# Optimization experiments

Hardware: AMD Instinct MI355X
Metric: run time of the kernel (lower is better)

The kernel has to match this reference:

```python
import jax, jax.numpy as jnp
import numpy as np

EPS = 1e-5

def conv2d(x, w, b):
    # x: [B,C,H,W], w: [O,I,kh,kw], VALID padding, stride 1
    y = jax.lax.conv_general_dilated(x, w, (1, 1), 'VALID',
                                     dimension_numbers=('NCHW', 'OIHW', 'NCHW'))
    return y + b[None, :, None, None]

def batchnorm(x, g, b):
    # training-mode BN: batch statistics over (N,H,W), biased variance (torch semantics)
    m = jnp.mean(x, axis=(0, 2, 3), keepdims=True)
    v = jnp.mean((x - m) ** 2, axis=(0, 2, 3), keepdims=True)
    return g[None, :, None, None] * (x - m) / jnp.sqrt(v + EPS) + b[None, :, None, None]

def maxpool2(x):
    return jax.lax.reduce_window(x, -jnp.inf, jax.lax.max,
                                 (1, 1, 2, 2), (1, 1, 2, 2), 'VALID')

def self_attention(x, qw, qb, kw, kb, vw, vb, gamma):
    # x: [B,C,H,W]; qw/kw: [C//8, C]; vw: [C, C] (1x1 convs)
    B, C, H, W = x.shape
    xf = x.reshape(B, C, H * W)                               # [B,C,N]
    q = jnp.einsum('oc,bcn->bon', qw, xf) + qb[None, :, None]  # [B,C//8,N]
    k = jnp.einsum('oc,bcn->bon', kw, xf) + kb[None, :, None]
    v = jnp.einsum('oc,bcn->bon', vw, xf) + vb[None, :, None]  # [B,C,N]
    energy = jnp.einsum('bcn,bcm->bnm', q, k)                  # [B,N,N] (query n, key m)
    attn = jax.nn.softmax(energy, axis=-1)
    out = jnp.einsum('bcm,bnm->bcn', v, attn)                  # [B,C,N]
    return gamma * out.reshape(B, C, H, W) + x

def setup_inputs() -> dict:
    key = jax.random.key(0)
    ks = jax.random.split(key, 20)
    s = 0.05
    d = {}
    d['x'] = jax.random.normal(ks[0], (1, 3, 256, 256), jnp.float32)
    d['conv1_w'] = jax.random.normal(ks[1], (32, 3, 3, 3), jnp.float32) * s
    d['conv1_b'] = jnp.zeros((32,), jnp.float32)
    d['bn1_g'] = jnp.ones((32,), jnp.float32)
    d['bn1_b'] = jnp.zeros((32,), jnp.float32)
    d['a1_qw'] = jax.random.normal(ks[2], (4, 32), jnp.float32) * s
    d['a1_qb'] = jnp.zeros((4,), jnp.float32)
    d['a1_kw'] = jax.random.normal(ks[3], (4, 32), jnp.float32) * s
    d['a1_kb'] = jnp.zeros((4,), jnp.float32)
    d['a1_vw'] = jax.random.normal(ks[4], (32, 32), jnp.float32) * s
    d['a1_vb'] = jnp.zeros((32,), jnp.float32)
    d['a1_gamma'] = jnp.ones((1,), jnp.float32)
    d['conv2_w'] = jax.random.normal(ks[5], (64, 32, 3, 3), jnp.float32) * s
    d['conv2_b'] = jnp.zeros((64,), jnp.float32)
    d['bn2_g'] = jnp.ones((64,), jnp.float32)
    d['bn2_b'] = jnp.zeros((64,), jnp.float32)
    d['a2_qw'] = jax.random.normal(ks[6], (8, 64), jnp.float32) * s
    d['a2_qb'] = jnp.zeros((8,), jnp.float32)
    d['a2_kw'] = jax.random.normal(ks[7], (8, 64), jnp.float32) * s
    d['a2_kb'] = jnp.zeros((8,), jnp.float32)
    d['a2_vw'] = jax.random.normal(ks[8], (64, 64), jnp.float32) * s
    d['a2_vb'] = jnp.zeros((64,), jnp.float32)
    d['a2_gamma'] = jnp.ones((1,), jnp.float32)
    d['fc_w'] = jax.random.normal(ks[9], (50, 64 * 62 * 62), jnp.float32) * 0.002
    d['fc_b'] = jnp.zeros((50,), jnp.float32)
    return d

def reference(x, conv1_w, conv1_b, bn1_g, bn1_b,
              a1_qw, a1_qb, a1_kw, a1_kb, a1_vw, a1_vb, a1_gamma,
              conv2_w, conv2_b, bn2_g, bn2_b,
              a2_qw, a2_qb, a2_kw, a2_kb, a2_vw, a2_vb, a2_gamma,
              fc_w, fc_b):
    h = conv2d(x, conv1_w, conv1_b)                 # [B,32,254,254]
    h = jax.nn.relu(batchnorm(h, bn1_g, bn1_b))
    h = maxpool2(h)                                 # [B,32,127,127]
    h = self_attention(h, a1_qw, a1_qb, a1_kw, a1_kb, a1_vw, a1_vb, a1_gamma)
    h = conv2d(h, conv2_w, conv2_b)                 # [B,64,125,125]
    h = jax.nn.relu(batchnorm(h, bn2_g, bn2_b))
    h = maxpool2(h)                                 # [B,64,62,62]
    h = self_attention(h, a2_qw, a2_qb, a2_kw, a2_kb, a2_vw, a2_vb, a2_gamma)
    h = h.reshape(h.shape[0], -1)                   # [B, 64*62*62]
    return h @ fc_w.T + fc_b
```

## Files before the change

### kernel.cpp

```cpp
#include <hip/hip_runtime.h>
#include <hip/hip_bf16.h>

typedef float f32x4 __attribute__((ext_vector_type(4)));
typedef short bf16x8 __attribute__((ext_vector_type(8)));

__device__ inline unsigned short f2bf(float x) {
    __hip_bfloat16 h = __float2bfloat16(x);
    return *reinterpret_cast<unsigned short*>(&h);
}

__global__ void conv3x3_kernel(const float* __restrict__ src, int Cin, int H, int W,
                               const float* __restrict__ w, const float* __restrict__ b,
                               float* __restrict__ dst, int OH, int OW) {
    extern __shared__ float lds[];
    float* xs = lds;
    float* ws = lds + Cin * 324;
    const int oc  = blockIdx.z;
    const int tx0 = blockIdx.x * 16, ty0 = blockIdx.y * 16;
    const int tid = threadIdx.y * 16 + threadIdx.x;

    for (int i = tid; i < Cin * 9; i += 256) ws[i] = w[oc * Cin * 9 + i];
    for (int i = tid; i < Cin * 324; i += 256) {
        int ic = i / 324;
        int r  = (i % 324) / 18;
        int cc = (i % 324) % 18;
        int y = ty0 + r, x = tx0 + cc;
        xs[i] = (y < H && x < W) ? src[((size_t)ic * H + y) * W + x] : 0.f;
    }
    __syncthreads();

    const int ox = tx0 + threadIdx.x, oy = ty0 + threadIdx.y;
    if (ox >= OW || oy >= OH) return;
    float acc = b[oc];
    for (int ic = 0; ic < Cin; ++ic) {
        const float* xp = &xs[ic * 324 + threadIdx.y * 18 + threadIdx.x];
        const float* wp = &ws[ic * 9];
        #pragma unroll
        for (int kh = 0; kh < 3; ++kh)
            #pragma unroll
            for (int kw = 0; kw < 3; ++kw)
                acc += xp[kh * 18 + kw] * wp[kh * 3 + kw];
    }
    dst[((size_t)oc * OH + oy) * OW + ox] = acc;
}

__global__ void bn_part_kernel(const float* __restrict__ src, int spatial,
                               float* __restrict__ part) {
    const int c = blockIdx.x, sb = blockIdx.y, SB = gridDim.y;
    const float* p = src + (size_t)c * spatial;
    const int nv4 = spatial >> 2;
    const int per = (nv4 + SB - 1) / SB;
    const int j0 = sb * per, j1 = min(nv4, j0 + per);
    float s = 0.f, sq = 0.f;
    const float4* p4 = (const float4*)p;
    for (int j = j0 + (int)threadIdx.x; j < j1; j += 256) {
        float4 x = p4[j];
        s  += x.x + x.y + x.z + x.w;
        sq += x.x * x.x + x.y * x.y + x.z * x.z + x.w * x.w;
    }
    if (sb == 0) {
        for (int j = (nv4 << 2) + (int)threadIdx.x; j < spatial; j += 256) {
            float x = p[j]; s += x; sq += x * x;
        }
    }
    __shared__ float rs[256], rq[256];
    rs[threadIdx.x] = s; rq[threadIdx.x] = sq;
    __syncthreads();
    for (int off = 128; off > 0; off >>= 1) {
        if ((int)threadIdx.x < off) {
            rs[threadIdx.x] += rs[threadIdx.x + off];
            rq[threadIdx.x] += rq[threadIdx.x + off];
        }
        __syncthreads();
    }
    if (threadIdx.x == 0) {
        part[(c * SB + sb) * 2]     = rs[0];
        part[(c * SB + sb) * 2 + 1] = rq[0];
    }
}

__global__ void bn_final_kernel(const float* __restrict__ part, int SB, int spatial,
                                const float* __restrict__ g, const float* __restrict__ bb,
                                float* __restrict__ inv_shift) {
    int c = blockIdx.x;
    if (threadIdx.x != 0) return;
    float s = 0.f, sq = 0.f;
    for (int i = 0; i < SB; ++i) {
        s  += part[(c * SB + i) * 2];
        sq += part[(c * SB + i) * 2 + 1];
    }
    float m   = s / (float)spatial;
    float var = sq / (float)spatial - m * m;
    float inv = g[c] * rsqrtf(var + 1e-5f);
    inv_shift[c * 2]     = inv;
    inv_shift[c * 2 + 1] = bb[c] - m * inv;
}

__global__ void bn_pool_kernel(const float* __restrict__ src,
                               const float* __restrict__ inv_shift,
                               int H, int W, int OH, int OW, int C,
                               float* __restrict__ dst) {
    int i = blockIdx.x * blockDim.x + threadIdx.x;
    if (i >= C * OH * OW) return;
    int ox = i % OW;
    int oy = (i / OW) % OH;
    int c  = i / (OW * OH);
    float inv = inv_shift[c * 2], sh = inv_shift[c * 2 + 1];
    const float* p = src + ((size_t)c * H + 2 * oy) * W + 2 * ox;
    float a = fmaxf(fmaf(p[0],     inv, sh), 0.f);
    float b = fmaxf(fmaf(p[1],     inv, sh), 0.f);
    float d = fmaxf(fmaf(p[W],     inv, sh), 0.f);
    float e = fmaxf(fmaf(p[W + 1], inv, sh), 0.f);
    dst[i] = fmaxf(fmaxf(a, b), fmaxf(d, e));
}

__global__ void qkv_proj_kernel(const float* __restrict__ xf, int N, int NP, int C, int Cqk,
                                const float* __restrict__ qw, const float* __restrict__ qb,
                                const float* __restrict__ kw, const float* __restrict__ kb,
                                const float* __restrict__ vw, const float* __restrict__ vb,
                                float* __restrict__ q, float* __restrict__ k,
                                unsigned short* __restrict__ v) {
    constexpr int OCG = 8;
    __shared__ float wl[OCG * 64 + OCG];
    const int g0 = blockIdx.y * OCG;
    const int tid = threadIdx.x;
    for (int i = tid; i < OCG * C; i += blockDim.x) {
        int o = i / C, cc = i % C;
        int oc = g0 + o;
        const float* wsrc = (oc < Cqk) ? (qw + oc * C)
                          : (oc < 2 * Cqk) ? (kw + (oc - Cqk) * C)
                          : (vw + (oc - 2 * Cqk) * C);
        wl[o * C + cc] = wsrc[cc];
    }
    if (tid < OCG) {
        int oc = g0 + tid;
        wl[OCG * C + tid] = (oc < Cqk) ? qb[oc]
                          : (oc < 2 * Cqk) ? kb[oc - Cqk]
                          : vb[oc - 2 * Cqk];
    }
    __syncthreads();
    int n = blockIdx.x * blockDim.x + tid;
    if (n >= N) return;
    float acc[OCG];
    #pragma unroll
    for (int o = 0; o < OCG; ++o) acc[o] = wl[OCG * C + o];
    for (int c = 0; c < C; ++c) {
        float xv = xf[(size_t)c * N + n];
        #pragma unroll
        for (int o = 0; o < OCG; ++o) acc[o] += xv * wl[o * C + c];
    }
    #pragma unroll
    for (int o = 0; o < OCG; ++o) {
        int oc = g0 + o;
        if (oc < Cqk)            q[(size_t)oc * NP + n] = acc[o];
        else if (oc < 2 * Cqk)   k[(size_t)(oc - Cqk) * NP + n] = acc[o];
        else                     v[(size_t)(oc - 2 * Cqk) * NP + n] = f2bf(acc[o]);
    }
}

template <int CQK, int CV>
__launch_bounds__(256)
__global__ void flash_mfma_kernel(const float* __restrict__ q,
                                  const float* __restrict__ k,
                                  const unsigned short* __restrict__ v,
                                  int N, int NP, int chunk,
                                  float* __restrict__ l_part,
                                  float* __restrict__ acc_part) {
    __shared__ float ksm[CQK * 32];
    __shared__ unsigned short vsm[CV * 32];
    const int tid  = threadIdx.x;
    const int wave = tid >> 6;
    const int lane = tid & 63;
    const int row  = lane & 15;
    const int g    = lane >> 4;
    const int s    = blockIdx.y;
    const int m0   = s * chunk;
    const int m1   = min(N, m0 + chunk);
    const int qb   = blockIdx.x * 64 + wave * 16;
    const int n    = qb + row;

    float qr[CQK];
    #pragma unroll
    for (int c = 0; c < CQK; ++c)
        qr[c] = (n < N) ? q[(size_t)c * NP + n] : 0.f;

    f32x4 acc[CV / 16];
    #pragma unroll
    for (int f = 0; f < CV / 16; ++f) acc[f] = (f32x4){0.f, 0.f, 0.f, 0.f};
    float lsum = 0.f;

    for (int mt = m0; mt < m1; mt += 32) {
        __syncthreads();
        for (int i = tid; i < CQK * 32; i += 256) {
            int c = i >> 5, kk = i & 31;
            int key = mt + kk;
            ksm[i] = (key < m1) ? k[(size_t)c * NP + key] : 0.f;
        }
        if (mt + 32 <= m1) {
            for (int i = tid * 4; i < CV * 32; i += 1024) {
                int ch = i >> 5, kk = i & 31;
                *(ushort4*)&vsm[i] = *(const ushort4*)&v[(size_t)ch * NP + mt + kk];
            }
        } else {
            for (int i = tid; i < CV * 32; i += 256) {
                int ch = i >> 5, kk = i & 31;
                int key = mt + kk;
                vsm[i] = (key < m1) ? v[(size_t)ch * NP + key] : (unsigned short)0;
            }
        }
        __syncthreads();

        float e[8];
        #pragma unroll
        for (int j = 0; j < 8; ++j) e[j] = 0.f;
        #pragma unroll
        for (int c = 0; c < CQK; ++c) {
            const float* kp = &ksm[c * 32 + 8 * g];
            #pragma unroll
            for (int j = 0; j < 8; ++j)
                e[j] = fmaf(qr[c], kp[j], e[j]);
        }
        bf16x8 pfrag;
        if (mt + 32 <= m1) {
            #pragma unroll
            for (int j = 0; j < 8; ++j) {
                float p = __expf(e[j]);
                lsum += p;
                pfrag[j] = (short)f2bf(p);
            }
        } else {
            #pragma unroll
            for (int j = 0; j < 8; ++j) {
                float p = (mt + 8 * g + j < m1) ? __expf(e[j]) : 0.f;
                lsum += p;
                pfrag[j] = (short)f2bf(p);
            }
        }
        #pragma unroll
        for (int f = 0; f < CV / 16; ++f) {
            bf16x8 vfrag = *(const bf16x8*)&vsm[(f * 16 + row) * 32 + 8 * g];
            acc[f] = __builtin_amdgcn_mfma_f32_16x16x32_bf16(pfrag, vfrag, acc[f], 0, 0, 0);
        }
    }

    lsum += __shfl_xor(lsum, 16, 64);
    lsum += __shfl_xor(lsum, 32, 64);
    if (g == 0 && n < N) l_part[(size_t)s * N + n] = lsum;

    #pragma unroll
    for (int f = 0; f < CV / 16; ++f) {
        #pragma unroll
        for (int r2 = 0; r2 < 4; ++r2) {
            int nq = qb + 4 * g + r2;
            if (nq < N)
                acc_part[((size_t)s * N + nq) * CV + f * 16 + row] = acc[f][r2];
        }
    }
}

__global__ void combine_kernel(const float* __restrict__ acc_part,
                               const float* __restrict__ l_part,
                               int nsplit, int N, int CV,
                               const float* __restrict__ gamma,
                               const float* __restrict__ x_res,
                               float* __restrict__ out) {
    int i = blockIdx.x * blockDim.x + threadIdx.x;
    if (i >= CV * N) return;
    int cv = i % CV;
    int n  = i / CV;
    float l = 0.f, a = 0.f;
    for (int s = 0; s < nsplit; ++s) l += l_part[(size_t)s * N + n];
    for (int s = 0; s < nsplit; ++s) a += acc_part[((size_t)s * N + n) * CV + cv];
    out[(size_t)cv * N + n] = gamma[0] * (a / l) + x_res[(size_t)cv * N + n];
}

__global__ void fc_partial_kernel(const float* __restrict__ h, const float* __restrict__ w,
                                  int K, int nchunk, float* __restrict__ partial) {
    const int r = blockIdx.y, cb = blockIdx.x;
    const int chunk = K / nchunk;
    const int j0 = cb * chunk;
    const int j1 = (cb == nchunk - 1) ? K : j0 + chunk;
    const float* wr = w + (size_t)r * K;
    float s = 0.f;
    for (int j = j0 + (int)threadIdx.x * 4; j + 3 < j1; j += blockDim.x * 4) {
        float4 hv = *reinterpret_cast<const float4*>(h + j);
        float4 wv = *reinterpret_cast<const float4*>(wr + j);
        s += hv.x * wv.x + hv.y * wv.y + hv.z * wv.z + hv.w * wv.w;
    }
    __shared__ float red[256];
    red[threadIdx.x] = s;
    __syncthreads();
    for (int off = 128; off > 0; off >>= 1) {
        if ((int)threadIdx.x < off) red[threadIdx.x] += red[threadIdx.x + off];
        __syncthreads();
    }
    if (threadIdx.x == 0) partial[r * gridDim.x + cb] = red[0];
}

__global__ void fc_final_kernel(const float* __restrict__ partial,
                                const float* __restrict__ b, int nchunk,
                                float* __restrict__ out) {
    int r = threadIdx.x;
    if (r < 50) {
        float s = b[r];
        for (int i = 0; i < nchunk; ++i) s += partial[r * nchunk + i];
        out[r] = s;
    }
}

extern "C" void kernel_launch(void* const* d_in, const int* in_sizes, int n_in,
                              void* d_out, int out_size, void* d_ws, size_t ws_size,
                              hipStream_t stream) {
    const float* x    = (const float*)d_in[0];
    const float* c1w  = (const float*)d_in[1];
    const float* c1b  = (const float*)d_in[2];
    const float* bn1g = (const float*)d_in[3];
    const float* bn1b = (const float*)d_in[4];
    const float* a1qw = (const float*)d_in[5];
    const float* a1qb = (const float*)d_in[6];
    const float* a1kw = (const float*)d_in[7];
    const float* a1kb = (const float*)d_in[8];
    const float* a1vw = (const float*)d_in[9];
    const float* a1vb = (const float*)d_in[10];
    const float* a1g  = (const float*)d_in[11];
    const float* c2w  = (const float*)d_in[12];
    const float* c2b  = (const float*)d_in[13];
    const float* bn2g = (const float*)d_in[14];
    const float* bn2b = (const float*)d_in[15];
    const float* a2qw = (const float*)d_in[16];
    const float* a2qb = (const float*)d_in[17];
    const float* a2kw = (const float*)d_in[18];
    const float* a2kb = (const float*)d_in[19];
    const float* a2vw = (const float*)d_in[20];
    const float* a2vb = (const float*)d_in[21];
    const float* a2g  = (const float*)d_in[22];
    const float* fcw  = (const float*)d_in[23];
    const float* fcb  = (const float*)d_in[24];
    float* out = (float*)d_out;

    const int N1 = 127 * 127;
    const int N2 = 62 * 62;
    const int NP1 = (N1 + 7) & ~7;
    const int NP2 = (N2 + 7) & ~7;
    const int NS1 = 8, NS2 = 16;

    char* base = (char*)d_ws;
    size_t off = 0;
    auto alloc = [&](size_t bytes) {
        void* p = base + off;
        off += (bytes + 63) & ~(size_t)63;
        return p;
    };
    float* h1   = (float*)alloc(sizeof(float) * 32 * 254 * 254);
    float* bnP  = (float*)alloc(sizeof(float) * 64 * 8 * 2);
    float* bnA  = (float*)alloc(sizeof(float) * 64);
    float* p1   = (float*)alloc(sizeof(float) * 32 * N1);
    float* q1   = (float*)alloc(sizeof(float) * 4 * NP1);
    float* k1   = (float*)alloc(sizeof(float) * 4 * NP1);
    unsigned short* v1 = (unsigned short*)alloc(sizeof(short) * 32 * NP1);
    float* l1   = (float*)alloc(sizeof(float) * NS1 * N1);
    float* a1p  = (float*)alloc(sizeof(float) * (size_t)NS1 * N1 * 32);
    float* ao1  = (float*)alloc(sizeof(float) * 32 * N1);
    float* h2   = (float*)alloc(sizeof(float) * 64 * 125 * 125);
    float* bnB  = (float*)alloc(sizeof(float) * 128);
    float* p2   = (float*)alloc(sizeof(float) * 64 * N2);
    float* q2   = (float*)alloc(sizeof(float) * 8 * NP2);
    float* k2   = (float*)alloc(sizeof(float) * 8 * NP2);
    unsigned short* v2 = (unsigned short*)alloc(sizeof(short) * 64 * NP2);
    float* l2   = (float*)alloc(sizeof(float) * NS2 * N2);
    float* a2p  = (float*)alloc(sizeof(float) * (size_t)NS2 * N2 * 64);
    float* ao2  = (float*)alloc(sizeof(float) * 64 * N2);
    float* fcp  = (float*)alloc(sizeof(float) * 512);

    {
        size_t smem = (3 * 324 + 3 * 9) * sizeof(float);
        conv3x3_kernel<<<dim3(16, 16, 32), dim3(16, 16), smem, stream>>>(
            x, 3, 256, 256, c1w, c1b, h1, 254, 254);
    }
    bn_part_kernel<<<dim3(32, 8), 256, 0, stream>>>(h1, 254 * 254, bnP);
    bn_final_kernel<<<32, 64, 0, stream>>>(bnP, 8, 254 * 254, bn1g, bn1b, bnA);
    bn_pool_kernel<<<(32 * N1 + 255) / 256, 256, 0, stream>>>(
        h1, bnA, 254, 254, 127, 127, 32, p1);

    qkv_proj_kernel<<<dim3((N1 + 255) / 256, 5), 256, 0, stream>>>(
        p1, N1, NP1, 32, 4, a1qw, a1qb, a1kw, a1kb, a1vw, a1vb, q1, k1, v1);
    {
        int chunk = (N1 + NS1 - 1) / NS1;
        flash_mfma_kernel<4, 32><<<dim3((N1 + 63) / 64, NS1), 256, 0, stream>>>(
            q1, k1, v1, N1, NP1, chunk, l1, a1p);
    }
    combine_kernel<<<(32 * N1 + 255) / 256, 256, 0, stream>>>(
        a1p, l1, NS1, N1, 32, a1g, p1, ao1);

    {
        size_t smem = (32 * 324 + 32 * 9) * sizeof(float);
        conv3x3_kernel<<<dim3(8, 8, 64), dim3(16, 16), smem, stream>>>(
            ao1, 32, 127, 127, c2w, c2b, h2, 125, 125);
    }
    bn_part_kernel<<<dim3(64, 8), 256, 0, stream>>>(h2, 125 * 125, bnP);
    bn_final_kernel<<<64, 64, 0, stream>>>(bnP, 8, 125 * 125, bn2g, bn2b, bnB);
    bn_pool_kernel<<<(64 * N2 + 255) / 256, 256, 0, stream>>>(
        h2, bnB, 125, 125, 62, 62, 64, p2);

    qkv_proj_kernel<<<dim3((N2 + 255) / 256, 10), 256, 0, stream>>>(
        p2, N2, NP2, 64, 8, a2qw, a2qb, a2kw, a2kb, a2vw, a2vb, q2, k2, v2);
    {
        int chunk = (N2 + NS2 - 1) / NS2;
        flash_mfma_kernel<8, 64><<<dim3((N2 + 63) / 64, NS2), 256, 0, stream>>>(
            q2, k2, v2, N2, NP2, chunk, l2, a2p);
    }
    combine_kernel<<<(64 * N2 + 255) / 256, 256, 0, stream>>>(
        a2p, l2, NS2, N2, 64, a2g, p2, ao2);

    fc_partial_kernel<<<dim3(8, 50), 256, 0, stream>>>(ao2, fcw, 64 * N2, 8, fcp);
    fc_final_kernel<<<1, 64, 0, stream>>>(fcp, fcb, 8, out);
}
```

Baseline: 275.8 us.

## Fuse BN stats into conv, stream K/V from global in flash kernel, vectorize combine

The conv kernel now reduces per-channel sum and sum of squares in shared memory and atomically adds them into a zeroed buffer, which removes the separate BN partial-reduction pass over the conv output. The flash attention kernel drops its shared-memory staging and barriers, reading K and V fragments straight from global memory with padded strides and 32-aligned chunks, and uses exp2 with log2e folded into q. The combine kernel is restructured to read contiguous 16-channel vectors per query, and the FC split count is raised. The atomics make the BN sums nondeterministic, and direct global loads in attention depend on cache reuse instead of explicit LDS sharing.

```diff
diff --git a/kernel.cpp b/kernel.cpp
--- a/kernel.cpp
+++ b/kernel.cpp
@@ -11,26 +11,32 @@
 
 __global__ void conv3x3_kernel(const float* __restrict__ src, int Cin, int H, int W,
                                const float* __restrict__ w, const float* __restrict__ b,
-                               float* __restrict__ dst, int OH, int OW) {
+                               float* __restrict__ dst, int OH, int OW,
+                               float* __restrict__ bn_accum) {
     extern __shared__ float lds[];
-    float* xs = lds;
-    float* ws = lds + Cin * 324;
+    float* xs  = lds;
+    float* ws  = lds + Cin * 324;
+    float* red = ws + Cin * 9;
     const int oc  = blockIdx.z;
     const int tx0 = blockIdx.x * 16, ty0 = blockIdx.y * 16;
     const int tid = threadIdx.y * 16 + threadIdx.x;
 
     for (int i = tid; i < Cin * 9; i += 256) ws[i] = w[oc * Cin * 9 + i];
-    for (int i = tid; i < Cin * 324; i += 256) {
-        int ic = i / 324;
-        int r  = (i % 324) / 18;
-        int cc = (i % 324) % 18;
-        int y = ty0 + r, x = tx0 + cc;
-        xs[i] = (y < H && x < W) ? src[((size_t)ic * H + y) * W + x] : 0.f;
+    {
+        int ic = 0, rem = tid;
+        for (int i = tid; i < Cin * 324; i += 256) {
+            int r  = rem / 18;
+            int cc = rem - r * 18;
+            int y = ty0 + r, x = tx0 + cc;
+            xs[i] = (y < H && x < W) ? src[((size_t)ic * H + y) * W + x] : 0.f;
+            rem += 256;
+            if (rem >= 324) { rem -= 324; ++ic; }
+        }
     }
     __syncthreads();
 
     const int ox = tx0 + threadIdx.x, oy = ty0 + threadIdx.y;
-    if (ox >= OW || oy >= OH) return;
+    const bool valid = (ox < OW && oy < OH);
     float acc = b[oc];
     for (int ic = 0; ic < Cin; ++ic) {
         const float* xp = &xs[ic * 324 + threadIdx.y * 18 + threadIdx.x];
@@ -39,58 +45,34 @@
         for (int kh = 0; kh < 3; ++kh)
             #pragma unroll
             for (int kw = 0; kw < 3; ++kw)
-                acc += xp[kh * 18 + kw] * wp[kh * 3 + kw];
-    }
-    dst[((size_t)oc * OH + oy) * OW + ox] = acc;
-}
-
-__global__ void bn_part_kernel(const float* __restrict__ src, int spatial,
-                               float* __restrict__ part) {
-    const int c = blockIdx.x, sb = blockIdx.y, SB = gridDim.y;
-    const float* p = src + (size_t)c * spatial;
-    const int nv4 = spatial >> 2;
-    const int per = (nv4 + SB - 1) / SB;
-    const int j0 = sb * per, j1 = min(nv4, j0 + per);
-    float s = 0.f, sq = 0.f;
-    const float4* p4 = (const float4*)p;
-    for (int j = j0 + (int)threadIdx.x; j < j1; j += 256) {
-        float4 x = p4[j];
-        s  += x.x + x.y + x.z + x.w;
-        sq += x.x * x.x + x.y * x.y + x.z * x.z + x.w * x.w;
-    }
-    if (sb == 0) {
-        for (int j = (nv4 << 2) + (int)threadIdx.x; j < spatial; j += 256) {
-            float x = p[j]; s += x; sq += x * x;
-        }
-    }
-    __shared__ float rs[256], rq[256];
-    rs[threadIdx.x] = s; rq[threadIdx.x] = sq;
+                acc = fmaf(xp[kh * 18 + kw], wp[kh * 3 + kw], acc);
+    }
+    if (valid) dst[((size_t)oc * OH + oy) * OW + ox] = acc;
+
+    float vs = valid ? acc : 0.f;
+    red[tid]       = vs;
+    red[256 + tid] = vs * vs;
     __syncthreads();
     for (int off = 128; off > 0; off >>= 1) {
-        if ((int)threadIdx.x < off) {
-            rs[threadIdx.x] += rs[threadIdx.x + off];
-            rq[threadIdx.x] += rq[threadIdx.x + off];
+        if (tid < off) {
+            red[tid]       += red[tid + off];
+            red[256 + tid] += red[256 + tid + off];
         }
         __syncthreads();
     }
-    if (threadIdx.x == 0) {
-        part[(c * SB + sb) * 2]     = rs[0];
-        part[(c * SB + sb) * 2 + 1] = rq[0];
-    }
-}
-
-__global__ void bn_final_kernel(const float* __restrict__ part, int SB, int spatial,
+    if (tid == 0) {
+        atomicAdd(&bn_accum[oc * 2],     red[0]);
+        atomicAdd(&bn_accum[oc * 2 + 1], red[256]);
+    }
+}
+
+__global__ void bn_final_kernel(const float* __restrict__ sums, int C, int spatial,
                                 const float* __restrict__ g, const float* __restrict__ bb,
                                 float* __restrict__ inv_shift) {
-    int c = blockIdx.x;
-    if (threadIdx.x != 0) return;
-    float s = 0.f, sq = 0.f;
-    for (int i = 0; i < SB; ++i) {
-        s  += part[(c * SB + i) * 2];
-        sq += part[(c * SB + i) * 2 + 1];
-    }
-    float m   = s / (float)spatial;
-    float var = sq / (float)spatial - m * m;
+    int c = threadIdx.x;
+    if (c >= C) return;
+    float m   = sums[c * 2] / (float)spatial;
+    float var = sums[c * 2 + 1] / (float)spatial - m * m;
     float inv = g[c] * rsqrtf(var + 1e-5f);
     inv_shift[c * 2]     = inv;
     inv_shift[c * 2 + 1] = bb[c] - m * inv;
@@ -147,7 +129,7 @@
     for (int c = 0; c < C; ++c) {
         float xv = xf[(size_t)c * N + n];
         #pragma unroll
-        for (int o = 0; o < OCG; ++o) acc[o] += xv * wl[o * C + c];
+        for (int o = 0; o < OCG; ++o) acc[o] = fmaf(xv, wl[o * C + c], acc[o]);
     }
     #pragma unroll
     for (int o = 0; o < OCG; ++o) {
@@ -166,8 +148,6 @@
                                   int N, int NP, int chunk,
                                   float* __restrict__ l_part,
                                   float* __restrict__ acc_part) {
-    __shared__ float ksm[CQK * 32];
-    __shared__ unsigned short vsm[CV * 32];
     const int tid  = threadIdx.x;
     const int wave = tid >> 6;
     const int lane = tid & 63;
@@ -182,64 +162,74 @@
     float qr[CQK];
     #pragma unroll
     for (int c = 0; c < CQK; ++c)
-        qr[c] = (n < N) ? q[(size_t)c * NP + n] : 0.f;
+        qr[c] = (n < N) ? q[(size_t)c * NP + n] * 1.44269504f : 0.f;
+
+    const float* kb[CQK];
+    #pragma unroll
+    for (int c = 0; c < CQK; ++c) kb[c] = k + (size_t)c * NP + 8 * g;
+    const unsigned short* vb[CV / 16];
+    #pragma unroll
+    for (int f = 0; f < CV / 16; ++f) vb[f] = v + (size_t)(f * 16 + row) * NP + 8 * g;
 
     f32x4 acc[CV / 16];
     #pragma unroll
     for (int f = 0; f < CV / 16; ++f) acc[f] = (f32x4){0.f, 0.f, 0.f, 0.f};
     float lsum = 0.f;
 
-    for (int mt = m0; mt < m1; mt += 32) {
-        __syncthreads();
-        for (int i = tid; i < CQK * 32; i += 256) {
-            int c = i >> 5, kk = i & 31;
-            int key = mt + kk;
-            ksm[i] = (key < m1) ? k[(size_t)c * NP + key] : 0.f;
-        }
-        if (mt + 32 <= m1) {
-            for (int i = tid * 4; i < CV * 32; i += 1024) {
-                int ch = i >> 5, kk = i & 31;
-                *(ushort4*)&vsm[i] = *(const ushort4*)&v[(size_t)ch * NP + mt + kk];
-            }
-        } else {
-            for (int i = tid; i < CV * 32; i += 256) {
-                int ch = i >> 5, kk = i & 31;
-                int key = mt + kk;
-                vsm[i] = (key < m1) ? v[(size_t)ch * NP + key] : (unsigned short)0;
-            }
-        }
-        __syncthreads();
-
-        float e[8];
-        #pragma unroll
-        for (int j = 0; j < 8; ++j) e[j] = 0.f;
+    const int nfull = (m1 - m0) & ~31;
+    int mt = m0;
+    for (; mt < m0 + nfull; mt += 32) {
+        f32x4 e0 = (f32x4){0.f, 0.f, 0.f, 0.f};
+        f32x4 e1 = (f32x4){0.f, 0.f, 0.f, 0.f};
         #pragma unroll
         for (int c = 0; c < CQK; ++c) {
-            const float* kp = &ksm[c * 32 + 8 * g];
-            #pragma unroll
-            for (int j = 0; j < 8; ++j)
-                e[j] = fmaf(qr[c], kp[j], e[j]);
+            f32x4 ka = *(const f32x4*)(kb[c] + mt);
+            f32x4 kc = *(const f32x4*)(kb[c] + mt + 4);
+            e0 += qr[c] * ka;
+            e1 += qr[c] * kc;
         }
         bf16x8 pfrag;
-        if (mt + 32 <= m1) {
-            #pragma unroll
-            for (int j = 0; j < 8; ++j) {
-                float p = __expf(e[j]);
-                lsum += p;
-                pfrag[j] = (short)f2bf(p);
-            }
-        } else {
-            #pragma unroll
-            for (int j = 0; j < 8; ++j) {
-                float p = (mt + 8 * g + j < m1) ? __expf(e[j]) : 0.f;
-                lsum += p;
-                pfrag[j] = (short)f2bf(p);
-            }
+        #pragma unroll
+        for (int j = 0; j < 4; ++j) {
+            float p = exp2f(e0[j]); lsum += p; pfrag[j] = (short)f2bf(p);
+        }
+        #pragma unroll
+        for (int j = 0; j < 4; ++j) {
+            float p = exp2f(e1[j]); lsum += p; pfrag[4 + j] = (short)f2bf(p);
         }
         #pragma unroll
         for (int f = 0; f < CV / 16; ++f) {
-            bf16x8 vfrag = *(const bf16x8*)&vsm[(f * 16 + row) * 32 + 8 * g];
-            acc[f] = __builtin_amdgcn_mfma_f32_16x16x32_bf16(pfrag, vfrag, acc[f], 0, 0, 0);
+            bf16x8 vf = *(const bf16x8*)(vb[f] + mt);
+            acc[f] = __builtin_amdgcn_mfma_f32_16x16x32_bf16(pfrag, vf, acc[f], 0, 0, 0);
+        }
+    }
+    if (mt < m1) {
+        f32x4 e0 = (f32x4){0.f, 0.f, 0.f, 0.f};
+        f32x4 e1 = (f32x4){0.f, 0.f, 0.f, 0.f};
+        #pragma unroll
+        for (int c = 0; c < CQK; ++c) {
+            f32x4 ka = *(const f32x4*)(kb[c] + mt);
+            f32x4 kc = *(const f32x4*)(kb[c] + mt + 4);
+            e0 += qr[c] * ka;
+            e1 += qr[c] * kc;
+        }
+        bf16x8 pfrag;
+        #pragma unroll
+        for (int j = 0; j < 4; ++j) {
+            bool ok = (mt + 8 * g + j) < m1;
+            float p = ok ? exp2f(e0[j]) : 0.f;
+            lsum += p; pfrag[j] = (short)f2bf(p);
+        }
+        #pragma unroll
+        for (int j = 0; j < 4; ++j) {
+            bool ok = (mt + 8 * g + 4 + j) < m1;
+            float p = ok ? exp2f(e1[j]) : 0.f;
+            lsum += p; pfrag[4 + j] = (short)f2bf(p);
+        }
+        #pragma unroll
+        for (int f = 0; f < CV / 16; ++f) {
+            bf16x8 vf = *(const bf16x8*)(vb[f] + mt);
+            acc[f] = __builtin_amdgcn_mfma_f32_16x16x32_bf16(pfrag, vf, acc[f], 0, 0, 0);
         }
     }
 
@@ -264,14 +254,27 @@
                                const float* __restrict__ gamma,
                                const float* __restrict__ x_res,
                                float* __restrict__ out) {
-    int i = blockIdx.x * blockDim.x + threadIdx.x;
-    if (i >= CV * N) return;
-    int cv = i % CV;
-    int n  = i / CV;
-    float l = 0.f, a = 0.f;
+    int n = blockIdx.x * blockDim.x + threadIdx.x;
+    if (n >= N) return;
+    int cv0 = blockIdx.y * 16;
+    float l = 0.f;
     for (int s = 0; s < nsplit; ++s) l += l_part[(size_t)s * N + n];
-    for (int s = 0; s < nsplit; ++s) a += acc_part[((size_t)s * N + n) * CV + cv];
-    out[(size_t)cv * N + n] = gamma[0] * (a / l) + x_res[(size_t)cv * N + n];
+    f32x4 a[4];
+    #pragma unroll
+    for (int t = 0; t < 4; ++t) a[t] = (f32x4){0.f, 0.f, 0.f, 0.f};
+    for (int s = 0; s < nsplit; ++s) {
+        const float* p = acc_part + ((size_t)s * N + n) * CV + cv0;
+        #pragma unroll
+        for (int t = 0; t < 4; ++t) a[t] += *(const f32x4*)(p + 4 * t);
+    }
+    float gs = gamma[0] / l;
+    #pragma unroll
+    for (int t = 0; t < 4; ++t)
+        #pragma unroll
+        for (int u = 0; u < 4; ++u) {
+            int cv = cv0 + 4 * t + u;
+            out[(size_t)cv * N + n] = fmaf(gs, a[t][u], x_res[(size_t)cv * N + n]);
+        }
 }
 
 __global__ void fc_partial_kernel(const float* __restrict__ h, const float* __restrict__ w,
@@ -340,9 +343,11 @@
 
     const int N1 = 127 * 127;
     const int N2 = 62 * 62;
-    const int NP1 = (N1 + 7) & ~7;
-    const int NP2 = (N2 + 7) & ~7;
+    const int NP1 = (N1 + 31) & ~31;
+    const int NP2 = (N2 + 31) & ~31;
     const int NS1 = 8, NS2 = 16;
+    const int CH1 = ((N1 + NS1 - 1) / NS1 + 31) & ~31;
+    const int CH2 = ((N2 + NS2 - 1) / NS2 + 31) & ~31;
 
     char* base = (char*)d_ws;
     size_t off = 0;
@@ -351,67 +356,61 @@
         off += (bytes + 63) & ~(size_t)63;
         return p;
     };
-    float* h1   = (float*)alloc(sizeof(float) * 32 * 254 * 254);
-    float* bnP  = (float*)alloc(sizeof(float) * 64 * 8 * 2);
-    float* bnA  = (float*)alloc(sizeof(float) * 64);
-    float* p1   = (float*)alloc(sizeof(float) * 32 * N1);
-    float* q1   = (float*)alloc(sizeof(float) * 4 * NP1);
-    float* k1   = (float*)alloc(sizeof(float) * 4 * NP1);
+    float* h1     = (float*)alloc(sizeof(float) * 32 * 254 * 254);
+    float* bnSums = (float*)alloc(sizeof(float) * 256);
+    float* bnA    = (float*)alloc(sizeof(float) * 64);
+    float* p1     = (float*)alloc(sizeof(float) * 32 * N1);
+    float* q1     = (float*)alloc(sizeof(float) * 4 * NP1);
+    float* k1     = (float*)alloc(sizeof(float) * 4 * NP1);
     unsigned short* v1 = (unsigned short*)alloc(sizeof(short) * 32 * NP1);
-    float* l1   = (float*)alloc(sizeof(float) * NS1 * N1);
-    float* a1p  = (float*)alloc(sizeof(float) * (size_t)NS1 * N1 * 32);
-    float* ao1  = (float*)alloc(sizeof(float) * 32 * N1);
-    float* h2   = (float*)alloc(sizeof(float) * 64 * 125 * 125);
-    float* bnB  = (float*)alloc(sizeof(float) * 128);
-    float* p2   = (float*)alloc(sizeof(float) * 64 * N2);
-    float* q2   = (float*)alloc(sizeof(float) * 8 * NP2);
-    float* k2   = (float*)alloc(sizeof(float) * 8 * NP2);
+    float* l1     = (float*)alloc(sizeof(float) * NS1 * N1);
+    float* a1p    = (float*)alloc(sizeof(float) * (size_t)NS1 * N1 * 32);
+    float* ao1    = (float*)alloc(sizeof(float) * 32 * N1);
+    float* h2     = (float*)alloc(sizeof(float) * 64 * 125 * 125);
+    float* bnB    = (float*)alloc(sizeof(float) * 128);
+    float* p2     = (float*)alloc(sizeof(float) * 64 * N2);
+    float* q2     = (float*)alloc(sizeof(float) * 8 * NP2);
+    float* k2     = (float*)alloc(sizeof(float) * 8 * NP2);
     unsigned short* v2 = (unsigned short*)alloc(sizeof(short) * 64 * NP2);
-    float* l2   = (float*)alloc(sizeof(float) * NS2 * N2);
-    float* a2p  = (float*)alloc(sizeof(float) * (size_t)NS2 * N2 * 64);
-    float* ao2  = (float*)alloc(sizeof(float) * 64 * N2);
-    float* fcp  = (float*)alloc(sizeof(float) * 512);
+    float* l2     = (float*)alloc(sizeof(float) * NS2 * N2);
+    float* a2p    = (float*)alloc(sizeof(float) * (size_t)NS2 * N2 * 64);
+    float* ao2    = (float*)alloc(sizeof(float) * 64 * N2);
+    float* fcp    = (float*)alloc(sizeof(float) * 2048);
+
+    hipMemsetAsync(bnSums, 0, 256 * sizeof(float), stream);
 
     {
-        size_t smem = (3 * 324 + 3 * 9) * sizeof(float);
+        size_t smem = (3 * 324 + 3 * 9 + 512) * sizeof(float);
         conv3x3_kernel<<<dim3(16, 16, 32), dim3(16, 16), smem, stream>>>(
-            x, 3, 256, 256, c1w, c1b, h1, 254, 254);
-    }
-    bn_part_kernel<<<dim3(32, 8), 256, 0, stream>>>(h1, 254 * 254, bnP);
-    bn_final_kernel<<<32, 64, 0, stream>>>(bnP, 8, 254 * 254, bn1g, bn1b, bnA);
+            x, 3, 256, 256, c1w, c1b, h1, 254, 254, bnSums);
+    }
+    bn_final_kernel<<<1, 32, 0, stream>>>(bnSums, 32, 254 * 254, bn1g, bn1b, bnA);
     bn_pool_kernel<<<(32 * N1 + 255) / 256, 256, 0, stream>>>(
         h1, bnA, 254, 254, 127, 127, 32, p1);
 
     qkv_proj_kernel<<<dim3((N1 + 255) / 256, 5), 256, 0, stream>>>(
         p1, N1, NP1, 32, 4, a1qw, a1qb, a1kw, a1kb, a1vw, a1vb, q1, k1, v1);
+    flash_mfma_kernel<4, 32><<<dim3((N1 + 63) / 64, NS1), 256, 0, stream>>>(
+        q1, k1, v1, N1, NP1, CH1, l1, a1p);
+    combine_kernel<<<dim3((N1 + 255) / 256, 2), 256, 0, stream>>>(
+        a1p, l1, NS1, N1, 32, a1g, p1, ao1);
+
     {
-        int chunk = (N1 + NS1 - 1) / NS1;
-        flash_mfma_kernel<4, 32><<<dim3((N1 + 63) / 64, NS1), 256, 0, stream>>>(
-            q1, k1, v1, N1, NP1, chunk, l1, a1p);
-    }
-    combine_kernel<<<(32 * N1 + 255) / 256, 256, 0, stream>>>(
-        a1p, l1, NS1, N1, 32, a1g, p1, ao1);
-
-    {
-        size_t smem = (32 * 324 + 32 * 9) * sizeof(float);
+        size_t smem = (32 * 324 + 32 * 9 + 512) * sizeof(float);
         conv3x3_kernel<<<dim3(8, 8, 64), dim3(16, 16), smem, stream>>>(
-            ao1, 32, 127, 127, c2w, c2b, h2, 125, 125);
-    }
-    bn_part_kernel<<<dim3(64, 8), 256, 0, stream>>>(h2, 125 * 125, bnP);
-    bn_final_kernel<<<64, 64, 0, stream>>>(bnP, 8, 125 * 125, bn2g, bn2b, bnB);
+            ao1, 32, 127, 127, c2w, c2b, h2, 125, 125, bnSums + 64);
+    }
+    bn_final_kernel<<<1, 64, 0, stream>>>(bnSums + 64, 64, 125 * 125, bn2g, bn2b, bnB);
     bn_pool_kernel<<<(64 * N2 + 255) / 256, 256, 0, stream>>>(
         h2, bnB, 125, 125, 62, 62, 64, p2);
 
     qkv_proj_kernel<<<dim3((N2 + 255) / 256, 10), 256, 0, stream>>>(
         p2, N2, NP2, 64, 8, a2qw, a2qb, a2kw, a2kb, a2vw, a2vb, q2, k2, v2);
-    {
-        int chunk = (N2 + NS2 - 1) / NS2;
-        flash_mfma_kernel<8, 64><<<dim3((N2 + 63) / 64, NS2), 256, 0, stream>>>(
-            q2, k2, v2, N2, NP2, chunk, l2, a2p);
-    }
-    combine_kernel<<<(64 * N2 + 255) / 256, 256, 0, stream>>>(
+    flash_mfma_kernel<8, 64><<<dim3((N2 + 63) / 64, NS2), 256, 0, stream>>>(
+        q2, k2, v2, N2, NP2, CH2, l2, a2p);
+    combine_kernel<<<dim3((N2 + 255) / 256, 4), 256, 0, stream>>>(
         a2p, l2, NS2, N2, 64, a2g, p2, ao2);
 
-    fc_partial_kernel<<<dim3(8, 50), 256, 0, stream>>>(ao2, fcw, 64 * N2, 8, fcp);
-    fc_final_kernel<<<1, 64, 0, stream>>>(fcp, fcb, 8, out);
-}
+    fc_partial_kernel<<<dim3(32, 50), 256, 0, stream>>>(ao2, fcw, 64 * N2, 32, fcp);
+    fc_final_kernel<<<1, 64, 0, stream>>>(fcp, fcb, 32, out);
+}
```

Result: slower. 605.0 us (+119.4%).
